# Kernel tuning notes

Measured on AMD Instinct MI355X. Metric: run time of the kernel, lower is better.

The kernel has to match this reference:

```python
import jax, jax.numpy as jnp
import numpy as np

TOP_P = 0.95        # sample() default topp
TEMPERATURE = 0.8   # token_temperature
NEG_INF = float('-inf')


def setup_inputs() -> dict:
    key = jax.random.key(0)
    k1, k2 = jax.random.split(key)
    B, V = 8192, 2048  # batch rows x speech-unit vocab
    logits = jax.random.normal(k1, (B, V), dtype=jnp.float32) * 4.0
    # uniform noise for Gumbel-max multinomial sampling (open interval)
    u = jax.random.uniform(k2, (B, V), dtype=jnp.float32, minval=1e-6, maxval=1.0 - 1e-6)
    return {"logits": logits, "u": u}


def _top_p_filter(logits, p):
    # descending sort (matches torch.sort(descending=True))
    order = jnp.argsort(-logits, axis=-1)                      # [B, V]
    sorted_logits = jnp.take_along_axis(logits, order, axis=-1)
    cum = jnp.cumsum(jax.nn.softmax(sorted_logits, axis=-1), axis=-1)
    remove = cum > p
    # shift right by one so the first token above the threshold is kept
    remove = jnp.concatenate(
        [jnp.zeros_like(remove[..., :1]), remove[..., :-1]], axis=-1)
    # scatter mask back to unsorted order via inverse permutation
    inv = jnp.argsort(order, axis=-1)
    remove_unsorted = jnp.take_along_axis(remove, inv, axis=-1)
    return jnp.where(remove_unsorted, NEG_INF, logits)


def reference(logits, u):
    scaled = logits / TEMPERATURE
    filtered = _top_p_filter(scaled, TOP_P)                    # [B, V]
    probs = jax.nn.softmax(filtered, axis=-1)                  # [B, V]
    # multinomial(probs, 1) == Gumbel-max over filtered logits
    gumbel = -jnp.log(-jnp.log(u))
    sampled = jnp.argmax(filtered + gumbel, axis=-1, keepdims=True)  # [B, 1]
    return sampled, probs
```

## Files before the change

kernel.cpp:

```cpp
#include <hip/hip_runtime.h>
#include <math.h>

#define VOCAB 2048
#define TPB   256
#define RPB   4
#define NBINS 64
#define BIN_SCALE 6.0f
#define CAP   512

typedef float vf4 __attribute__((ext_vector_type(4)));

__global__ __launch_bounds__(TPB, 4) void sampler_kernel(
    const float* __restrict__ logits,
    const float* __restrict__ uni,
    float* __restrict__ out_idx,
    float* __restrict__ out_probs)
{
    const int lane = threadIdx.x & 63;
    const int wid  = threadIdx.x >> 6;
    const int row  = (blockIdx.x << 2) | wid;

    __shared__ float s_bins[RPB][NBINS];
    __shared__ float s_cv[RPB][CAP];
    __shared__ float s_ci[RPB][CAP];
    __shared__ int   s_bcnt[RPB];
    __shared__ int   s_kcnt[RPB];

    const float* lrow = logits    + (size_t)row * VOCAB;
    const float* urow = uni       + (size_t)row * VOCAB;
    float*       prow = out_probs + (size_t)row * VOCAB;

    s_bins[wid][lane] = 0.0f;
    if (lane == 0) { s_bcnt[wid] = 0; s_kcnt[wid] = 0; }

    float s[32];
    #pragma unroll
    for (int j = 0; j < 8; j++) {
        vf4 a = __builtin_nontemporal_load((const vf4*)(lrow + j * 256 + 4 * lane));
        s[4*j+0] = a.x * 1.25f;
        s[4*j+1] = a.y * 1.25f;
        s[4*j+2] = a.z * 1.25f;
        s[4*j+3] = a.w * 1.25f;
    }

    float m0 = s[0], m1 = s[1], m2 = s[2], m3 = s[3];
    #pragma unroll
    for (int j = 4; j < 32; j += 4) {
        m0 = fmaxf(m0, s[j+0]); m1 = fmaxf(m1, s[j+1]);
        m2 = fmaxf(m2, s[j+2]); m3 = fmaxf(m3, s[j+3]);
    }
    float m = fmaxf(fmaxf(m0, m1), fmaxf(m2, m3));
    #pragma unroll
    for (int off = 32; off; off >>= 1)
        m = fmaxf(m, __shfl_xor(m, off));

    float e[32];
    double p0 = 0.0, p1 = 0.0;
    #pragma unroll
    for (int j = 0; j < 32; j++) {
        e[j] = __expf(s[j] - m);
        if (j & 1) p1 += (double)e[j]; else p0 += (double)e[j];
        int b = (int)((m - s[j]) * BIN_SCALE);
        if (b < NBINS) atomicAdd(&s_bins[wid][b], e[j]);
    }
    double dp = p0 + p1;
    #pragma unroll
    for (int off = 32; off; off >>= 1)
        dp += __shfl_xor(dp, off);
    const double S  = dp;
    const double pS = 0.95 * S;

    const float bf = s_bins[wid][lane];
    double c = (double)bf;
    #pragma unroll
    for (int d = 1; d < 64; d <<= 1) {
        double o = __shfl_up(c, d);
        if (lane >= d) c += o;
    }
    const unsigned long long ball = __ballot(c > pS);
    const int bstar = ball ? (__ffsll(ball) - 1) : (NBINS - 1);
    double excl = c - (double)bf;
    const double cumBefore = __shfl(excl, bstar);

    #pragma unroll
    for (int j = 0; j < 32; j++) {
        int b = (int)((m - s[j]) * BIN_SCALE);
        if (b == bstar) {
            int pos = atomicAdd(&s_bcnt[wid], 1);
            if (pos < CAP) { s_cv[wid][pos] = s[j]; s_ci[wid][pos] = e[j]; }
        }
    }
    const int bcnt = min(s_bcnt[wid], CAP);

    unsigned keptMask = 0;
    float k0 = 0.0f, k1 = 0.0f;
    #pragma unroll
    for (int j = 0; j < 32; j++) {
        int b = (int)((m - s[j]) * BIN_SCALE);
        bool kept;
        if (b < bstar)      kept = true;
        else if (b > bstar) kept = false;
        else {
            float part = 0.0f;
            for (int i = 0; i < bcnt; i++)
                if (s_cv[wid][i] > s[j]) part += s_ci[wid][i];
            kept = (cumBefore + (double)part) <= pS;
        }
        if (kept) {
            keptMask |= (1u << j);
            if (j & 1) k1 += e[j]; else k0 += e[j];
        }
    }
    float kpsum = k0 + k1;
    #pragma unroll
    for (int off = 32; off; off >>= 1)
        kpsum += __shfl_xor(kpsum, off);
    const float invSK = 1.0f / kpsum;

    #pragma unroll
    for (int j = 0; j < 8; j++) {
        vf4 p;
        p.x = ((keptMask >> (4*j+0)) & 1u) ? e[4*j+0] * invSK : 0.0f;
        p.y = ((keptMask >> (4*j+1)) & 1u) ? e[4*j+1] * invSK : 0.0f;
        p.z = ((keptMask >> (4*j+2)) & 1u) ? e[4*j+2] * invSK : 0.0f;
        p.w = ((keptMask >> (4*j+3)) & 1u) ? e[4*j+3] * invSK : 0.0f;
        __builtin_nontemporal_store(p, (vf4*)(prow + j * 256 + 4 * lane));
    }

    unsigned ovf = 0;
    #pragma unroll
    for (int j = 0; j < 32; j++) {
        if ((keptMask >> j) & 1u) {
            int pos = atomicAdd(&s_kcnt[wid], 1);
            if (pos < CAP) {
                s_cv[wid][pos] = s[j];
                s_ci[wid][pos] = __int_as_float((j >> 2) * 256 + 4 * lane + (j & 3));
            } else {
                ovf |= (1u << j);
            }
        }
    }
    const int kc = min(s_kcnt[wid], CAP);

    unsigned long long key = 0ull;
    for (int i = lane; i < kc; i += 64) {
        float sv  = s_cv[wid][i];
        int   idx = __float_as_int(s_ci[wid][i]);
        float uv  = urow[idx];
        float g   = -logf(-logf(uv));
        float z   = sv + g;
        unsigned zb = __float_as_uint(z);
        zb = (zb & 0x80000000u) ? ~zb : (zb | 0x80000000u);
        unsigned long long kk =
            ((unsigned long long)zb << 32) | (unsigned)(VOCAB - 1 - idx);
        key = (kk > key) ? kk : key;
    }
    if (__builtin_expect(ovf != 0, 0)) {
        #pragma unroll
        for (int j = 0; j < 32; j++) {
            if ((ovf >> j) & 1u) {
                int   idx = (j >> 2) * 256 + 4 * lane + (j & 3);
                float uv  = urow[idx];
                float g   = -logf(-logf(uv));
                float z   = s[j] + g;
                unsigned zb = __float_as_uint(z);
                zb = (zb & 0x80000000u) ? ~zb : (zb | 0x80000000u);
                unsigned long long kk =
                    ((unsigned long long)zb << 32) | (unsigned)(VOCAB - 1 - idx);
                key = (kk > key) ? kk : key;
            }
        }
    }
    #pragma unroll
    for (int off = 32; off; off >>= 1) {
        unsigned long long ok = __shfl_xor(key, off);
        key = (ok > key) ? ok : key;
    }
    if (lane == 0)
        out_idx[row] = (float)(VOCAB - 1 - (int)(key & 0xFFFFFFFFu));
}

extern "C" void kernel_launch(void* const* d_in, const int* in_sizes, int n_in,
                              void* d_out, int out_size, void* d_ws, size_t ws_size,
                              hipStream_t stream) {
    const float* logits = (const float*)d_in[0];
    const float* u      = (const float*)d_in[1];
    const int B = in_sizes[0] / VOCAB;
    float* out_idx   = (float*)d_out;
    float* out_probs = (float*)d_out + B;
    sampler_kernel<<<B / RPB, TPB, 0, stream>>>(logits, u, out_idx, out_probs);
}
```

Before: 169.7 us.

## Process two rows per wavefront with both rows' logits loaded up front

```diff
diff --git a/kernel.cpp b/kernel.cpp
--- a/kernel.cpp
+++ b/kernel.cpp
@@ -3,7 +3,8 @@
 
 #define VOCAB 2048
 #define TPB   256
-#define RPB   4
+#define WPB   4
+#define RPW   2
 #define NBINS 64
 #define BIN_SCALE 6.0f
 #define CAP   512
@@ -18,166 +19,182 @@
 {
     const int lane = threadIdx.x & 63;
     const int wid  = threadIdx.x >> 6;
-    const int row  = (blockIdx.x << 2) | wid;
-
-    __shared__ float s_bins[RPB][NBINS];
-    __shared__ float s_cv[RPB][CAP];
-    __shared__ float s_ci[RPB][CAP];
-    __shared__ int   s_bcnt[RPB];
-    __shared__ int   s_kcnt[RPB];
-
-    const float* lrow = logits    + (size_t)row * VOCAB;
-    const float* urow = uni       + (size_t)row * VOCAB;
-    float*       prow = out_probs + (size_t)row * VOCAB;
-
-    s_bins[wid][lane] = 0.0f;
-    if (lane == 0) { s_bcnt[wid] = 0; s_kcnt[wid] = 0; }
-
-    float s[32];
+    const int gw   = blockIdx.x * WPB + wid;
+    const int r0   = gw * RPW;
+
+    __shared__ float s_bins[WPB][NBINS];
+    __shared__ float s_cv[WPB][CAP];
+    __shared__ float s_ci[WPB][CAP];
+    __shared__ int   s_bcnt[WPB];
+    __shared__ int   s_kcnt[WPB];
+
+    const float* l0 = logits + (size_t)r0 * VOCAB;
+    vf4 b0[8], b1[8];
     #pragma unroll
-    for (int j = 0; j < 8; j++) {
-        vf4 a = __builtin_nontemporal_load((const vf4*)(lrow + j * 256 + 4 * lane));
-        s[4*j+0] = a.x * 1.25f;
-        s[4*j+1] = a.y * 1.25f;
-        s[4*j+2] = a.z * 1.25f;
-        s[4*j+3] = a.w * 1.25f;
+    for (int j = 0; j < 8; j++)
+        b0[j] = __builtin_nontemporal_load((const vf4*)(l0 + j * 256 + 4 * lane));
+    #pragma unroll
+    for (int j = 0; j < 8; j++)
+        b1[j] = __builtin_nontemporal_load((const vf4*)(l0 + VOCAB + j * 256 + 4 * lane));
+
+    #pragma unroll
+    for (int rr = 0; rr < RPW; rr++) {
+        const int row = r0 + rr;
+        const float* urow = uni       + (size_t)row * VOCAB;
+        float*       prow = out_probs + (size_t)row * VOCAB;
+
+        s_bins[wid][lane] = 0.0f;
+        if (lane == 0) { s_bcnt[wid] = 0; s_kcnt[wid] = 0; }
+
+        float s[32];
+        #pragma unroll
+        for (int j = 0; j < 8; j++) {
+            vf4 a = (rr == 0) ? b0[j] : b1[j];
+            s[4*j+0] = a.x * 1.25f;
+            s[4*j+1] = a.y * 1.25f;
+            s[4*j+2] = a.z * 1.25f;
+            s[4*j+3] = a.w * 1.25f;
+        }
+
+        float m0 = s[0], m1 = s[1], m2 = s[2], m3 = s[3];
+        #pragma unroll
+        for (int j = 4; j < 32; j += 4) {
+            m0 = fmaxf(m0, s[j+0]); m1 = fmaxf(m1, s[j+1]);
+            m2 = fmaxf(m2, s[j+2]); m3 = fmaxf(m3, s[j+3]);
+        }
+        float m = fmaxf(fmaxf(m0, m1), fmaxf(m2, m3));
+        #pragma unroll
+        for (int off = 32; off; off >>= 1)
+            m = fmaxf(m, __shfl_xor(m, off));
+
+        double p0 = 0.0, p1 = 0.0;
+        #pragma unroll
+        for (int j = 0; j < 32; j++) {
+            float e = __expf(s[j] - m);
+            if (j & 1) p1 += (double)e; else p0 += (double)e;
+            int b = (int)((m - s[j]) * BIN_SCALE);
+            if (b < NBINS) atomicAdd(&s_bins[wid][b], e);
+        }
+        double dp = p0 + p1;
+        #pragma unroll
+        for (int off = 32; off; off >>= 1)
+            dp += __shfl_xor(dp, off);
+        const double S  = dp;
+        const double pS = 0.95 * S;
+
+        const float bf = s_bins[wid][lane];
+        double c = (double)bf;
+        #pragma unroll
+        for (int d = 1; d < 64; d <<= 1) {
+            double o = __shfl_up(c, d);
+            if (lane >= d) c += o;
+        }
+        const unsigned long long ball = __ballot(c > pS);
+        const int bstar = ball ? (__ffsll(ball) - 1) : (NBINS - 1);
+        double excl = c - (double)bf;
+        const double cumBefore = __shfl(excl, bstar);
+
+        #pragma unroll
+        for (int j = 0; j < 32; j++) {
+            int b = (int)((m - s[j]) * BIN_SCALE);
+            if (b == bstar) {
+                int pos = atomicAdd(&s_bcnt[wid], 1);
+                if (pos < CAP) {
+                    s_cv[wid][pos] = s[j];
+                    s_ci[wid][pos] = __expf(s[j] - m);
+                }
+            }
+        }
+        const int bcnt = min(s_bcnt[wid], CAP);
+
+        unsigned keptMask = 0;
+        float k0 = 0.0f, k1 = 0.0f;
+        #pragma unroll
+        for (int j = 0; j < 32; j++) {
+            int b = (int)((m - s[j]) * BIN_SCALE);
+            bool kept;
+            if (b < bstar)      kept = true;
+            else if (b > bstar) kept = false;
+            else {
+                float part = 0.0f;
+                for (int i = 0; i < bcnt; i++)
+                    if (s_cv[wid][i] > s[j]) part += s_ci[wid][i];
+                kept = (cumBefore + (double)part) <= pS;
+            }
+            if (kept) {
+                keptMask |= (1u << j);
+                float e = __expf(s[j] - m);
+                if (j & 1) k1 += e; else k0 += e;
+            }
+        }
+        float kpsum = k0 + k1;
+        #pragma unroll
+        for (int off = 32; off; off >>= 1)
+            kpsum += __shfl_xor(kpsum, off);
+        const float invSK = 1.0f / kpsum;
+
+        #pragma unroll
+        for (int j = 0; j < 8; j++) {
+            vf4 p;
+            p.x = ((keptMask >> (4*j+0)) & 1u) ? __expf(s[4*j+0] - m) * invSK : 0.0f;
+            p.y = ((keptMask >> (4*j+1)) & 1u) ? __expf(s[4*j+1] - m) * invSK : 0.0f;
+            p.z = ((keptMask >> (4*j+2)) & 1u) ? __expf(s[4*j+2] - m) * invSK : 0.0f;
+            p.w = ((keptMask >> (4*j+3)) & 1u) ? __expf(s[4*j+3] - m) * invSK : 0.0f;
+            __builtin_nontemporal_store(p, (vf4*)(prow + j * 256 + 4 * lane));
+        }
+
+        unsigned ovf = 0;
+        #pragma unroll
+        for (int j = 0; j < 32; j++) {
+            if ((keptMask >> j) & 1u) {
+                int pos = atomicAdd(&s_kcnt[wid], 1);
+                if (pos < CAP) {
+                    s_cv[wid][pos] = s[j];
+                    s_ci[wid][pos] = __int_as_float((j >> 2) * 256 + 4 * lane + (j & 3));
+                } else {
+                    ovf |= (1u << j);
+                }
+            }
+        }
+        const int kc = min(s_kcnt[wid], CAP);
+
+        unsigned long long key = 0ull;
+        for (int i = lane; i < kc; i += 64) {
+            float sv  = s_cv[wid][i];
+            int   idx = __float_as_int(s_ci[wid][i]);
+            float uv  = urow[idx];
+            float g   = -logf(-logf(uv));
+            float z   = sv + g;
+            unsigned zb = __float_as_uint(z);
+            zb = (zb & 0x80000000u) ? ~zb : (zb | 0x80000000u);
+            unsigned long long kk =
+                ((unsigned long long)zb << 32) | (unsigned)(VOCAB - 1 - idx);
+            key = (kk > key) ? kk : key;
+        }
+        if (__builtin_expect(ovf != 0, 0)) {
+            #pragma unroll
+            for (int j = 0; j < 32; j++) {
+                if ((ovf >> j) & 1u) {
+                    int   idx = (j >> 2) * 256 + 4 * lane + (j & 3);
+                    float uv  = urow[idx];
+                    float g   = -logf(-logf(uv));
+                    float z   = s[j] + g;
+                    unsigned zb = __float_as_uint(z);
+                    zb = (zb & 0x80000000u) ? ~zb : (zb | 0x80000000u);
+                    unsigned long long kk =
+                        ((unsigned long long)zb << 32) | (unsigned)(VOCAB - 1 - idx);
+                    key = (kk > key) ? kk : key;
+                }
+            }
+        }
+        #pragma unroll
+        for (int off = 32; off; off >>= 1) {
+            unsigned long long ok = __shfl_xor(key, off);
+            key = (ok > key) ? ok : key;
+        }
+        if (lane == 0)
+            out_idx[row] = (float)(VOCAB - 1 - (int)(key & 0xFFFFFFFFu));
     }
-
-    float m0 = s[0], m1 = s[1], m2 = s[2], m3 = s[3];
-    #pragma unroll
-    for (int j = 4; j < 32; j += 4) {
-        m0 = fmaxf(m0, s[j+0]); m1 = fmaxf(m1, s[j+1]);
-        m2 = fmaxf(m2, s[j+2]); m3 = fmaxf(m3, s[j+3]);
-    }
-    float m = fmaxf(fmaxf(m0, m1), fmaxf(m2, m3));
-    #pragma unroll
-    for (int off = 32; off; off >>= 1)
-        m = fmaxf(m, __shfl_xor(m, off));
-
-    float e[32];
-    double p0 = 0.0, p1 = 0.0;
-    #pragma unroll
-    for (int j = 0; j < 32; j++) {
-        e[j] = __expf(s[j] - m);
-        if (j & 1) p1 += (double)e[j]; else p0 += (double)e[j];
-        int b = (int)((m - s[j]) * BIN_SCALE);
-        if (b < NBINS) atomicAdd(&s_bins[wid][b], e[j]);
-    }
-    double dp = p0 + p1;
-    #pragma unroll
-    for (int off = 32; off; off >>= 1)
-        dp += __shfl_xor(dp, off);
-    const double S  = dp;
-    const double pS = 0.95 * S;
-
-    const float bf = s_bins[wid][lane];
-    double c = (double)bf;
-    #pragma unroll
-    for (int d = 1; d < 64; d <<= 1) {
-        double o = __shfl_up(c, d);
-        if (lane >= d) c += o;
-    }
-    const unsigned long long ball = __ballot(c > pS);
-    const int bstar = ball ? (__ffsll(ball) - 1) : (NBINS - 1);
-    double excl = c - (double)bf;
-    const double cumBefore = __shfl(excl, bstar);
-
-    #pragma unroll
-    for (int j = 0; j < 32; j++) {
-        int b = (int)((m - s[j]) * BIN_SCALE);
-        if (b == bstar) {
-            int pos = atomicAdd(&s_bcnt[wid], 1);
-            if (pos < CAP) { s_cv[wid][pos] = s[j]; s_ci[wid][pos] = e[j]; }
-        }
-    }
-    const int bcnt = min(s_bcnt[wid], CAP);
-
-    unsigned keptMask = 0;
-    float k0 = 0.0f, k1 = 0.0f;
-    #pragma unroll
-    for (int j = 0; j < 32; j++) {
-        int b = (int)((m - s[j]) * BIN_SCALE);
-        bool kept;
-        if (b < bstar)      kept = true;
-        else if (b > bstar) kept = false;
-        else {
-            float part = 0.0f;
-            for (int i = 0; i < bcnt; i++)
-                if (s_cv[wid][i] > s[j]) part += s_ci[wid][i];
-            kept = (cumBefore + (double)part) <= pS;
-        }
-        if (kept) {
-            keptMask |= (1u << j);
-            if (j & 1) k1 += e[j]; else k0 += e[j];
-        }
-    }
-    float kpsum = k0 + k1;
-    #pragma unroll
-    for (int off = 32; off; off >>= 1)
-        kpsum += __shfl_xor(kpsum, off);
-    const float invSK = 1.0f / kpsum;
-
-    #pragma unroll
-    for (int j = 0; j < 8; j++) {
-        vf4 p;
-        p.x = ((keptMask >> (4*j+0)) & 1u) ? e[4*j+0] * invSK : 0.0f;
-        p.y = ((keptMask >> (4*j+1)) & 1u) ? e[4*j+1] * invSK : 0.0f;
-        p.z = ((keptMask >> (4*j+2)) & 1u) ? e[4*j+2] * invSK : 0.0f;
-        p.w = ((keptMask >> (4*j+3)) & 1u) ? e[4*j+3] * invSK : 0.0f;
-        __builtin_nontemporal_store(p, (vf4*)(prow + j * 256 + 4 * lane));
-    }
-
-    unsigned ovf = 0;
-    #pragma unroll
-    for (int j = 0; j < 32; j++) {
-        if ((keptMask >> j) & 1u) {
-            int pos = atomicAdd(&s_kcnt[wid], 1);
-            if (pos < CAP) {
-                s_cv[wid][pos] = s[j];
-                s_ci[wid][pos] = __int_as_float((j >> 2) * 256 + 4 * lane + (j & 3));
-            } else {
-                ovf |= (1u << j);
-            }
-        }
-    }
-    const int kc = min(s_kcnt[wid], CAP);
-
-    unsigned long long key = 0ull;
-    for (int i = lane; i < kc; i += 64) {
-        float sv  = s_cv[wid][i];
-        int   idx = __float_as_int(s_ci[wid][i]);
-        float uv  = urow[idx];
-        float g   = -logf(-logf(uv));
-        float z   = sv + g;
-        unsigned zb = __float_as_uint(z);
-        zb = (zb & 0x80000000u) ? ~zb : (zb | 0x80000000u);
-        unsigned long long kk =
-            ((unsigned long long)zb << 32) | (unsigned)(VOCAB - 1 - idx);
-        key = (kk > key) ? kk : key;
-    }
-    if (__builtin_expect(ovf != 0, 0)) {
-        #pragma unroll
-        for (int j = 0; j < 32; j++) {
-            if ((ovf >> j) & 1u) {
-                int   idx = (j >> 2) * 256 + 4 * lane + (j & 3);
-                float uv  = urow[idx];
-                float g   = -logf(-logf(uv));
-                float z   = s[j] + g;
-                unsigned zb = __float_as_uint(z);
-                zb = (zb & 0x80000000u) ? ~zb : (zb | 0x80000000u);
-                unsigned long long kk =
-                    ((unsigned long long)zb << 32) | (unsigned)(VOCAB - 1 - idx);
-                key = (kk > key) ? kk : key;
-            }
-        }
-    }
-    #pragma unroll
-    for (int off = 32; off; off >>= 1) {
-        unsigned long long ok = __shfl_xor(key, off);
-        key = (ok > key) ? ok : key;
-    }
-    if (lane == 0)
-        out_idx[row] = (float)(VOCAB - 1 - (int)(key & 0xFFFFFFFFu));
 }
 
 extern "C" void kernel_launch(void* const* d_in, const int* in_sizes, int n_in,
@@ -188,5 +205,5 @@
     const int B = in_sizes[0] / VOCAB;
     float* out_idx   = (float*)d_out;
     float* out_probs = (float*)d_out + B;
-    sampler_kernel<<<B / RPB, TPB, 0, stream>>>(logits, u, out_idx, out_probs);
+    sampler_kernel<<<B / (WPB * RPW), TPB, 0, stream>>>(logits, u, out_idx, out_probs);
 }
```

New measurement: 185.9 us. +9.6%, slower.

## Process multiple rows per wave with async global-to-LDS prefetch of next row

Applied to the files above, without the earlier changes.

```diff
diff --git a/kernel.cpp b/kernel.cpp
--- a/kernel.cpp
+++ b/kernel.cpp
@@ -3,14 +3,15 @@
 
 #define VOCAB 2048
 #define TPB   256
-#define RPB   4
+#define WPB   4
+#define RPW   4
 #define NBINS 64
 #define BIN_SCALE 6.0f
-#define CAP   512
+#define CAP   256
 
 typedef float vf4 __attribute__((ext_vector_type(4)));
 
-__global__ __launch_bounds__(TPB, 4) void sampler_kernel(
+__global__ __launch_bounds__(TPB, 2) void sampler_kernel(
     const float* __restrict__ logits,
     const float* __restrict__ uni,
     float* __restrict__ out_idx,
@@ -18,166 +19,201 @@
 {
     const int lane = threadIdx.x & 63;
     const int wid  = threadIdx.x >> 6;
-    const int row  = (blockIdx.x << 2) | wid;
-
-    __shared__ float s_bins[RPB][NBINS];
-    __shared__ float s_cv[RPB][CAP];
-    __shared__ float s_ci[RPB][CAP];
-    __shared__ int   s_bcnt[RPB];
-    __shared__ int   s_kcnt[RPB];
-
-    const float* lrow = logits    + (size_t)row * VOCAB;
-    const float* urow = uni       + (size_t)row * VOCAB;
-    float*       prow = out_probs + (size_t)row * VOCAB;
-
-    s_bins[wid][lane] = 0.0f;
-    if (lane == 0) { s_bcnt[wid] = 0; s_kcnt[wid] = 0; }
-
-    float s[32];
+    const int base = (blockIdx.x * WPB + wid) * RPW;
+
+    __shared__ float s_stage[WPB][VOCAB];
+    __shared__ float s_bins[WPB][NBINS];
+    __shared__ float s_cv[WPB][CAP];
+    __shared__ float s_ci[WPB][CAP];
+    __shared__ int   s_bcnt[WPB];
+    __shared__ int   s_kcnt[WPB];
+
+    const float* lbase = logits + (size_t)base * VOCAB;
+
+    vf4 b[8];
     #pragma unroll
-    for (int j = 0; j < 8; j++) {
-        vf4 a = __builtin_nontemporal_load((const vf4*)(lrow + j * 256 + 4 * lane));
-        s[4*j+0] = a.x * 1.25f;
-        s[4*j+1] = a.y * 1.25f;
-        s[4*j+2] = a.z * 1.25f;
-        s[4*j+3] = a.w * 1.25f;
+    for (int j = 0; j < 8; j++)
+        b[j] = __builtin_nontemporal_load((const vf4*)(lbase + j * 256 + 4 * lane));
+    #pragma unroll
+    for (int j = 0; j < 8; j++)
+        __builtin_amdgcn_global_load_lds(
+            (const __attribute__((address_space(1))) void*)(lbase + VOCAB + j * 256 + 4 * lane),
+            (__attribute__((address_space(3))) void*)(&s_stage[wid][j * 256]),
+            16, 0, 0);
+
+    #pragma unroll 1
+    for (int rr = 0; rr < RPW; rr++) {
+        const int row = base + rr;
+        const float* urow = uni       + (size_t)row * VOCAB;
+        float*       prow = out_probs + (size_t)row * VOCAB;
+
+        s_bins[wid][lane] = 0.0f;
+        if (lane == 0) { s_bcnt[wid] = 0; s_kcnt[wid] = 0; }
+
+        float s[32];
+        #pragma unroll
+        for (int j = 0; j < 8; j++) {
+            s[4*j+0] = b[j].x * 1.25f;
+            s[4*j+1] = b[j].y * 1.25f;
+            s[4*j+2] = b[j].z * 1.25f;
+            s[4*j+3] = b[j].w * 1.25f;
+        }
+
+        float m0 = s[0], m1 = s[1], m2 = s[2], m3 = s[3];
+        #pragma unroll
+        for (int j = 4; j < 32; j += 4) {
+            m0 = fmaxf(m0, s[j+0]); m1 = fmaxf(m1, s[j+1]);
+            m2 = fmaxf(m2, s[j+2]); m3 = fmaxf(m3, s[j+3]);
+        }
+        float m = fmaxf(fmaxf(m0, m1), fmaxf(m2, m3));
+        #pragma unroll
+        for (int off = 32; off; off >>= 1)
+            m = fmaxf(m, __shfl_xor(m, off));
+
+        float e[32];
+        double p0 = 0.0, p1 = 0.0;
+        #pragma unroll
+        for (int j = 0; j < 32; j++) {
+            e[j] = __expf(s[j] - m);
+            if (j & 1) p1 += (double)e[j]; else p0 += (double)e[j];
+            int bb = (int)((m - s[j]) * BIN_SCALE);
+            if (bb < NBINS) atomicAdd(&s_bins[wid][bb], e[j]);
+        }
+        double dp = p0 + p1;
+        #pragma unroll
+        for (int off = 32; off; off >>= 1)
+            dp += __shfl_xor(dp, off);
+        const double S  = dp;
+        const double pS = 0.95 * S;
+
+        const float bf = s_bins[wid][lane];
+        double c = (double)bf;
+        #pragma unroll
+        for (int d = 1; d < 64; d <<= 1) {
+            double o = __shfl_up(c, d);
+            if (lane >= d) c += o;
+        }
+        const unsigned long long ball = __ballot(c > pS);
+        const int bstar = ball ? (__ffsll(ball) - 1) : (NBINS - 1);
+        double excl = c - (double)bf;
+        const double cumBefore = __shfl(excl, bstar);
+
+        #pragma unroll
+        for (int j = 0; j < 32; j++) {
+            int bb = (int)((m - s[j]) * BIN_SCALE);
+            if (bb == bstar) {
+                int pos = atomicAdd(&s_bcnt[wid], 1);
+                if (pos < CAP) { s_cv[wid][pos] = s[j]; s_ci[wid][pos] = e[j]; }
+            }
+        }
+        const int bcnt = min(s_bcnt[wid], CAP);
+
+        unsigned keptMask = 0;
+        float k0 = 0.0f, k1 = 0.0f;
+        #pragma unroll
+        for (int j = 0; j < 32; j++) {
+            int bb = (int)((m - s[j]) * BIN_SCALE);
+            bool kept;
+            if (bb < bstar)      kept = true;
+            else if (bb > bstar) kept = false;
+            else {
+                float part = 0.0f;
+                for (int i = 0; i < bcnt; i++)
+                    if (s_cv[wid][i] > s[j]) part += s_ci[wid][i];
+                kept = (cumBefore + (double)part) <= pS;
+            }
+            if (kept) {
+                keptMask |= (1u << j);
+                if (j & 1) k1 += e[j]; else k0 += e[j];
+            }
+        }
+        float kpsum = k0 + k1;
+        #pragma unroll
+        for (int off = 32; off; off >>= 1)
+            kpsum += __shfl_xor(kpsum, off);
+        const float invSK = 1.0f / kpsum;
+
+        #pragma unroll
+        for (int j = 0; j < 8; j++) {
+            vf4 p;
+            p.x = ((keptMask >> (4*j+0)) & 1u) ? e[4*j+0] * invSK : 0.0f;
+            p.y = ((keptMask >> (4*j+1)) & 1u) ? e[4*j+1] * invSK : 0.0f;
+            p.z = ((keptMask >> (4*j+2)) & 1u) ? e[4*j+2] * invSK : 0.0f;
+            p.w = ((keptMask >> (4*j+3)) & 1u) ? e[4*j+3] * invSK : 0.0f;
+            __builtin_nontemporal_store(p, (vf4*)(prow + j * 256 + 4 * lane));
+        }
+
+        unsigned ovf = 0;
+        #pragma unroll
+        for (int j = 0; j < 32; j++) {
+            if ((keptMask >> j) & 1u) {
+                int pos = atomicAdd(&s_kcnt[wid], 1);
+                if (pos < CAP) {
+                    s_cv[wid][pos] = s[j];
+                    s_ci[wid][pos] = __int_as_float((j >> 2) * 256 + 4 * lane + (j & 3));
+                } else {
+                    ovf |= (1u << j);
+                }
+            }
+        }
+        const int kc = min(s_kcnt[wid], CAP);
+
+        unsigned long long key = 0ull;
+        for (int i = lane; i < kc; i += 64) {
+            float sv  = s_cv[wid][i];
+            int   idx = __float_as_int(s_ci[wid][i]);
+            float uv  = urow[idx];
+            float g   = -logf(-logf(uv));
+            float z   = sv + g;
+            unsigned zb = __float_as_uint(z);
+            zb = (zb & 0x80000000u) ? ~zb : (zb | 0x80000000u);
+            unsigned long long kk =
+                ((unsigned long long)zb << 32) | (unsigned)(VOCAB - 1 - idx);
+            key = (kk > key) ? kk : key;
+        }
+        if (__builtin_expect(ovf != 0, 0)) {
+            #pragma unroll
+            for (int j = 0; j < 32; j++) {
+                if ((ovf >> j) & 1u) {
+                    int   idx = (j >> 2) * 256 + 4 * lane + (j & 3);
+                    float uv  = urow[idx];
+                    float g   = -logf(-logf(uv));
+                    float z   = s[j] + g;
+                    unsigned zb = __float_as_uint(z);
+                    zb = (zb & 0x80000000u) ? ~zb : (zb | 0x80000000u);
+                    unsigned long long kk =
+                        ((unsigned long long)zb << 32) | (unsigned)(VOCAB - 1 - idx);
+                    key = (kk > key) ? kk : key;
+                }
+            }
+        }
+        #pragma unroll
+        for (int off = 32; off; off >>= 1) {
+            unsigned long long ok = __shfl_xor(key, off);
+            key = (ok > key) ? ok : key;
+        }
+        if (lane == 0)
+            out_idx[row] = (float)(VOCAB - 1 - (int)(key & 0xFFFFFFFFu));
+
+        if (rr + 1 < RPW) {
+            asm volatile("s_waitcnt vmcnt(0)" ::: "memory");
+            __builtin_amdgcn_sched_barrier(0);
+            #pragma unroll
+            for (int j = 0; j < 8; j++)
+                b[j] = *(const vf4*)(&s_stage[wid][j * 256 + 4 * lane]);
+            asm volatile("s_waitcnt lgkmcnt(0)" ::: "memory");
+            __builtin_amdgcn_sched_barrier(0);
+            if (rr + 2 < RPW) {
+                const float* nsrc = lbase + (size_t)(rr + 2) * VOCAB;
+                #pragma unroll
+                for (int j = 0; j < 8; j++)
+                    __builtin_amdgcn_global_load_lds(
+                        (const __attribute__((address_space(1))) void*)(nsrc + j * 256 + 4 * lane),
+                        (__attribute__((address_space(3))) void*)(&s_stage[wid][j * 256]),
+                        16, 0, 0);
+            }
+        }
     }
-
-    float m0 = s[0], m1 = s[1], m2 = s[2], m3 = s[3];
-    #pragma unroll
-    for (int j = 4; j < 32; j += 4) {
-        m0 = fmaxf(m0, s[j+0]); m1 = fmaxf(m1, s[j+1]);
-        m2 = fmaxf(m2, s[j+2]); m3 = fmaxf(m3, s[j+3]);
-    }
-    float m = fmaxf(fmaxf(m0, m1), fmaxf(m2, m3));
-    #pragma unroll
-    for (int off = 32; off; off >>= 1)
-        m = fmaxf(m, __shfl_xor(m, off));
-
-    float e[32];
-    double p0 = 0.0, p1 = 0.0;
-    #pragma unroll
-    for (int j = 0; j < 32; j++) {
-        e[j] = __expf(s[j] - m);
-        if (j & 1) p1 += (double)e[j]; else p0 += (double)e[j];
-        int b = (int)((m - s[j]) * BIN_SCALE);
-        if (b < NBINS) atomicAdd(&s_bins[wid][b], e[j]);
-    }
-    double dp = p0 + p1;
-    #pragma unroll
-    for (int off = 32; off; off >>= 1)
-        dp += __shfl_xor(dp, off);
-    const double S  = dp;
-    const double pS = 0.95 * S;
-
-    const float bf = s_bins[wid][lane];
-    double c = (double)bf;
-    #pragma unroll
-    for (int d = 1; d < 64; d <<= 1) {
-        double o = __shfl_up(c, d);
-        if (lane >= d) c += o;
-    }
-    const unsigned long long ball = __ballot(c > pS);
-    const int bstar = ball ? (__ffsll(ball) - 1) : (NBINS - 1);
-    double excl = c - (double)bf;
-    const double cumBefore = __shfl(excl, bstar);
-
-    #pragma unroll
-    for (int j = 0; j < 32; j++) {
-        int b = (int)((m - s[j]) * BIN_SCALE);
-        if (b == bstar) {
-            int pos = atomicAdd(&s_bcnt[wid], 1);
-            if (pos < CAP) { s_cv[wid][pos] = s[j]; s_ci[wid][pos] = e[j]; }
-        }
-    }
-    const int bcnt = min(s_bcnt[wid], CAP);
-
-    unsigned keptMask = 0;
-    float k0 = 0.0f, k1 = 0.0f;
-    #pragma unroll
-    for (int j = 0; j < 32; j++) {
-        int b = (int)((m - s[j]) * BIN_SCALE);
-        bool kept;
-        if (b < bstar)      kept = true;
-        else if (b > bstar) kept = false;
-        else {
-            float part = 0.0f;
-            for (int i = 0; i < bcnt; i++)
-                if (s_cv[wid][i] > s[j]) part += s_ci[wid][i];
-            kept = (cumBefore + (double)part) <= pS;
-        }
-        if (kept) {
-            keptMask |= (1u << j);
-            if (j & 1) k1 += e[j]; else k0 += e[j];
-        }
-    }
-    float kpsum = k0 + k1;
-    #pragma unroll
-    for (int off = 32; off; off >>= 1)
-        kpsum += __shfl_xor(kpsum, off);
-    const float invSK = 1.0f / kpsum;
-
-    #pragma unroll
-    for (int j = 0; j < 8; j++) {
-        vf4 p;
-        p.x = ((keptMask >> (4*j+0)) & 1u) ? e[4*j+0] * invSK : 0.0f;
-        p.y = ((keptMask >> (4*j+1)) & 1u) ? e[4*j+1] * invSK : 0.0f;
-        p.z = ((keptMask >> (4*j+2)) & 1u) ? e[4*j+2] * invSK : 0.0f;
-        p.w = ((keptMask >> (4*j+3)) & 1u) ? e[4*j+3] * invSK : 0.0f;
-        __builtin_nontemporal_store(p, (vf4*)(prow + j * 256 + 4 * lane));
-    }
-
-    unsigned ovf = 0;
-    #pragma unroll
-    for (int j = 0; j < 32; j++) {
-        if ((keptMask >> j) & 1u) {
-            int pos = atomicAdd(&s_kcnt[wid], 1);
-            if (pos < CAP) {
-                s_cv[wid][pos] = s[j];
-                s_ci[wid][pos] = __int_as_float((j >> 2) * 256 + 4 * lane + (j & 3));
-            } else {
-                ovf |= (1u << j);
-            }
-        }
-    }
-    const int kc = min(s_kcnt[wid], CAP);
-
-    unsigned long long key = 0ull;
-    for (int i = lane; i < kc; i += 64) {
-        float sv  = s_cv[wid][i];
-        int   idx = __float_as_int(s_ci[wid][i]);
-        float uv  = urow[idx];
-        float g   = -logf(-logf(uv));
-        float z   = sv + g;
-        unsigned zb = __float_as_uint(z);
-        zb = (zb & 0x80000000u) ? ~zb : (zb | 0x80000000u);
-        unsigned long long kk =
-            ((unsigned long long)zb << 32) | (unsigned)(VOCAB - 1 - idx);
-        key = (kk > key) ? kk : key;
-    }
-    if (__builtin_expect(ovf != 0, 0)) {
-        #pragma unroll
-        for (int j = 0; j < 32; j++) {
-            if ((ovf >> j) & 1u) {
-                int   idx = (j >> 2) * 256 + 4 * lane + (j & 3);
-                float uv  = urow[idx];
-                float g   = -logf(-logf(uv));
-                float z   = s[j] + g;
-                unsigned zb = __float_as_uint(z);
-                zb = (zb & 0x80000000u) ? ~zb : (zb | 0x80000000u);
-                unsigned long long kk =
-                    ((unsigned long long)zb << 32) | (unsigned)(VOCAB - 1 - idx);
-                key = (kk > key) ? kk : key;
-            }
-        }
-    }
-    #pragma unroll
-    for (int off = 32; off; off >>= 1) {
-        unsigned long long ok = __shfl_xor(key, off);
-        key = (ok > key) ? ok : key;
-    }
-    if (lane == 0)
-        out_idx[row] = (float)(VOCAB - 1 - (int)(key & 0xFFFFFFFFu));
 }
 
 extern "C" void kernel_launch(void* const* d_in, const int* in_sizes, int n_in,
@@ -188,5 +224,5 @@
     const int B = in_sizes[0] / VOCAB;
     float* out_idx   = (float*)d_out;
     float* out_probs = (float*)d_out + B;
-    sampler_kernel<<<B / RPB, TPB, 0, stream>>>(logits, u, out_idx, out_probs);
+    sampler_kernel<<<B / (WPB * RPW), TPB, 0, stream>>>(logits, u, out_idx, out_probs);
 }
```

Result: slower. 181.7 us (+7.1%).
